# Performance work log

Measured on AMD Instinct MI355X. Metric: run time of the kernel, lower is better.

Reference implementation:

```python
import jax, jax.numpy as jnp
import numpy as np

B, T, D_HID, D_TRK, N_TRANS = 128, 40, 512, 256, 64


def setup_inputs() -> dict:
    key = jax.random.key(0)
    ks = jax.random.split(key, 8)
    d, t = D_HID, D_TRK
    s = 0.05
    return {
        "buffers": jax.random.normal(ks[0], (B, T, 2 * d), jnp.float32),
        "W_left": jax.random.normal(ks[1], (5 * d, d), jnp.float32) * s,
        "b_left": jnp.zeros((5 * d,), jnp.float32),
        "W_right": jax.random.normal(ks[2], (5 * d, d), jnp.float32) * s,
        "W_track": jax.random.normal(ks[3], (5 * d, t), jnp.float32) * s,
        "W_ih": jax.random.normal(ks[4], (4 * t, 3 * d), jnp.float32) * s,
        "W_hh": jax.random.normal(ks[5], (4 * t, t), jnp.float32) * s,
        "b_ih": jnp.zeros((4 * t,), jnp.float32),
        "b_hh": jnp.zeros((4 * t,), jnp.float32),
        "W_trans": jax.random.normal(ks[6], (4, t), jnp.float32) * s,
        "b_trans": jnp.zeros((4,), jnp.float32),
        "transitions": jax.random.randint(ks[7], (N_TRANS, B), 0, 4),
    }


def _spinn_forward(buffers, W_left, b_left, W_right, W_track,
                   W_ih, W_hh, b_ih, b_hh, W_trans, b_trans, n_steps):
    # Thin-stack style vectorized SPINN: fixed-capacity stack + pointers.
    Bb, Tt, two_d = buffers.shape
    d = two_d // 2
    t = W_hh.shape[1]
    cap = Tt + 2  # stack never exceeds 2 initial + (T-2) shifts
    dtype = buffers.dtype

    stack0 = jnp.zeros((Bb, cap, two_d), dtype)
    # stacks = [buf[0], buf[0]] in the torch code
    stack0 = stack0.at[:, 0].set(buffers[:, 0]).at[:, 1].set(buffers[:, 0])
    sptr0 = jnp.full((Bb,), 2, jnp.int32)   # stack length
    blen0 = jnp.full((Bb,), Tt, jnp.int32)  # buffer length (pops from the end)
    th0 = jnp.zeros((Bb, t), dtype)
    tc0 = jnp.zeros((Bb, t), dtype)
    bidx = jnp.arange(Bb)

    def step(carry, _):
        stack, sptr, blen, th, tc = carry
        buf_top = buffers[bidx, blen - 1]          # buf[-1], [B, 2d]
        s1 = stack[bidx, sptr - 1]                 # stack[-1]
        s2 = stack[bidx, sptr - 2]                 # stack[-2]
        # Tracker LSTMCell on cat(buf_h, stack1_h, stack2_h)
        x = jnp.concatenate([buf_top[:, :d], s1[:, :d], s2[:, :d]], axis=1)
        gates = x @ W_ih.T + b_ih + th @ W_hh.T + b_hh
        gi, gf, gg, go = jnp.split(gates, 4, axis=1)
        tc_new = jax.nn.sigmoid(gf) * tc + jax.nn.sigmoid(gi) * jnp.tanh(gg)
        th_new = jax.nn.sigmoid(go) * jnp.tanh(tc_new)
        logits = th_new @ W_trans.T + b_trans      # [B, 4]
        trans = jnp.argmax(logits, axis=1)
        do_shift = (trans == 3) & (blen > 2)
        do_red = (trans == 2) & (sptr > 3)
        # REDUCE (TreeLSTM) computed for all rows, masked in below.
        # left = stack[-2], right = stack[-1] (right popped first in torch).
        lstm_in = (s2[:, :d] @ W_left.T + b_left
                   + s1[:, :d] @ W_right.T
                   + th_new @ W_track.T)           # [B, 5d]
        a, i_, f1, f2, o_ = jnp.split(lstm_in, 5, axis=1)
        c = (jnp.tanh(a) * jax.nn.sigmoid(i_)
             + jax.nn.sigmoid(f1) * s2[:, d:]
             + jax.nn.sigmoid(f2) * s1[:, d:])
        h = jax.nn.sigmoid(o_) * jnp.tanh(c)
        node = jnp.concatenate([h, c], axis=1)
        # SHIFT: push buf_top; REDUCE: overwrite stack[-2] and shrink by 1.
        stack = stack.at[bidx, sptr].set(
            jnp.where(do_shift[:, None], buf_top, stack[bidx, sptr]))
        stack = stack.at[bidx, sptr - 2].set(
            jnp.where(do_red[:, None], node, stack[bidx, sptr - 2]))
        sptr = sptr + do_shift.astype(jnp.int32) - do_red.astype(jnp.int32)
        blen = blen - do_shift.astype(jnp.int32)
        return (stack, sptr, blen, th_new, tc_new), logits

    _, all_logits = jax.lax.scan(step, (stack0, sptr0, blen0, th0, tc0),
                                 None, length=n_steps)
    return all_logits  # [n_steps, B, 4] = stacked trans_preds_batch


def reference(buffers, W_left, b_left, W_right, W_track, W_ih, W_hh,
              b_ih, b_hh, W_trans, b_trans, transitions):
    n_steps = transitions.shape[0]  # torch only uses transitions.size(0)
    return _spinn_forward(buffers, W_left, b_left, W_right, W_track,
                          W_ih, W_hh, b_ih, b_hh, W_trans, b_trans, n_steps)
```

## Files before the change

### kernel.cpp

```cpp
#include <hip/hip_runtime.h>
#include <math.h>


#define B_ 128
#define CAP 40
#define XW 1536
#define GSPLIT 12
#define LSPLIT 8
#define NSTEP 64

__device__ __forceinline__ float sigm(float x) { return 1.f / (1.f + expf(-x)); }

__global__ void k_repack(const float* __restrict__ W_ih, const float* __restrict__ W_hh,
                         const float* __restrict__ W_left, const float* __restrict__ W_right,
                         const float* __restrict__ W_track, const float* __restrict__ b_ih,
                         const float* __restrict__ b_hh,
                         float* __restrict__ W1T, float* __restrict__ W2T,
                         float* __restrict__ W3T, float* __restrict__ WhhT,
                         float* __restrict__ b1) {
    size_t idx = (size_t)blockIdx.x * 256 + threadIdx.x;
    const size_t n1 = 1536ull * 1024ull;
    const size_t n2 = 1024ull * 2560ull;
    const size_t n3 = 256ull * 2560ull;
    const size_t n4 = 256ull * 1024ull;
    if (idx < n1) {
        int k = (int)(idx >> 10), n = (int)(idx & 1023);
        W1T[idx] = W_ih[(size_t)n * 1536 + k];
    } else if (idx < n1 + n2) {
        size_t r = idx - n1;
        int k = (int)(r / 2560), n = (int)(r % 2560);
        W2T[r] = (k < 512) ? W_right[(size_t)n * 512 + k] : W_left[(size_t)n * 512 + (k - 512)];
    } else if (idx < n1 + n2 + n3) {
        size_t r = idx - n1 - n2;
        int k = (int)(r / 2560), n = (int)(r % 2560);
        W3T[r] = W_track[(size_t)n * 256 + k];
    } else if (idx < n1 + n2 + n3 + n4) {
        size_t r = idx - n1 - n2 - n3;
        int k = (int)(r >> 10), n = (int)(r & 1023);
        WhhT[r] = W_hh[(size_t)n * 256 + k];
    } else if (idx < n1 + n2 + n3 + n4 + 1024) {
        int i = (int)(idx - n1 - n2 - n3 - n4);
        b1[i] = b_ih[i] + b_hh[i];
    }
}

__global__ void k_init(const float* __restrict__ buffers, float* __restrict__ stack,
                       float* __restrict__ X, float* __restrict__ tc,
                       float* __restrict__ hh,
                       int* __restrict__ sptr, int* __restrict__ blen) {
    int b = blockIdx.x, t = threadIdx.x;
    const float* b0 = buffers + (size_t)b * 40 * 1024;
    const float* btop = b0 + 39 * 1024;
    float* stk = stack + (size_t)b * CAP * 1024;
    for (int j = t; j < 1024; j += 256) { stk[j] = b0[j]; stk[1024 + j] = b0[j]; }
    float* Xb = X + (size_t)b * XW;
    for (int j = t; j < 512; j += 256) {
        Xb[j] = btop[j]; Xb[512 + j] = b0[j]; Xb[1024 + j] = b0[j];
    }
    tc[b * 256 + t] = 0.f;
    for (int j = t; j < 1024; j += 256) hh[(size_t)b * 1024 + j] = 0.f;
    if (t == 0) { sptr[b] = 2; blen[b] = 40; }
}

__global__ __launch_bounds__(256, 3) void k_gemm(const float* __restrict__ X,
                                                 const float* __restrict__ W1T,
                                                 const float* __restrict__ W2T,
                                                 float* __restrict__ gpart,
                                                 float* __restrict__ lpart) {
    __shared__ float As[32][132];
    __shared__ float Ws[32][68];
    const int bid = blockIdx.x;
    const float* WT; float* out; int N, n0, k0, aoff;
    if (bid < 192) {
        int ks = bid >> 4, nb = bid & 15;
        WT = W1T; out = gpart + (size_t)ks * 131072;
        N = 1024; n0 = nb * 64; k0 = ks * 128; aoff = 0;
    } else {
        int tI = bid - 192; int ks = tI / 40, nb = tI % 40;
        WT = W2T; out = lpart + (size_t)ks * 327680;
        N = 2560; n0 = nb * 64; k0 = ks * 128; aoff = 512;
    }
    const int tid = threadIdx.x;
    const int tm = tid >> 4;
    const int tn = tid & 15;

    float acc[8][4];
#pragma unroll
    for (int i = 0; i < 8; i++)
#pragma unroll
        for (int j = 0; j < 4; j++) acc[i][j] = 0.f;

    for (int ki = 0; ki < 128; ki += 32) {
        const int kb = k0 + ki;
        __syncthreads();
        {
            int m = tid >> 1;
            int c8 = (tid & 1) * 16;
            const float4* src = (const float4*)(X + (size_t)m * XW + aoff + kb + c8);
#pragma unroll
            for (int j = 0; j < 4; j++) {
                float4 v = src[j];
                int kk = c8 + j * 4;
                As[kk + 0][m] = v.x; As[kk + 1][m] = v.y; As[kk + 2][m] = v.z; As[kk + 3][m] = v.w;
            }
        }
        {
            int kk = tid >> 3;
            int c = (tid & 7) * 8;
            const float4* src = (const float4*)(WT + (size_t)(kb + kk) * N + n0 + c);
            float4* dst = (float4*)(&Ws[kk][c]);
            dst[0] = src[0]; dst[1] = src[1];
        }
        __syncthreads();
#pragma unroll 4
        for (int kk = 0; kk < 32; kk++) {
            float a[8], w[4];
            *(float4*)&a[0] = *(const float4*)&As[kk][tm * 4];
            *(float4*)&a[4] = *(const float4*)&As[kk][64 + tm * 4];
            *(float4*)&w[0] = *(const float4*)&Ws[kk][tn * 4];
#pragma unroll
            for (int i = 0; i < 8; i++)
#pragma unroll
                for (int j = 0; j < 4; j++) acc[i][j] += a[i] * w[j];
        }
    }
    float* base = out + n0 + tn * 4;
#pragma unroll
    for (int i = 0; i < 8; i++) {
        int m = (i < 4) ? (tm * 4 + i) : (64 + tm * 4 + (i - 4));
        *(float4*)(base + (size_t)m * N) = make_float4(acc[i][0], acc[i][1], acc[i][2], acc[i][3]);
    }
}

__global__ __launch_bounds__(256) void k_B(const float* __restrict__ gpart,
                                           const float* __restrict__ lpart,
                                           const float* __restrict__ hh_in,
                                           float* __restrict__ hh_out,
                                           const float* __restrict__ b1,
                                           const float* __restrict__ b_left,
                                           const float* __restrict__ W3T,
                                           const float* __restrict__ WhhT,
                                           const float* __restrict__ W_trans,
                                           const float* __restrict__ b_trans,
                                           const float* __restrict__ buffers,
                                           float* __restrict__ stack,
                                           float* __restrict__ X,
                                           const float* __restrict__ tc_in,
                                           float* __restrict__ tc_out,
                                           const int* __restrict__ sp_in,
                                           int* __restrict__ sp_out,
                                           const int* __restrict__ bl_in,
                                           int* __restrict__ bl_out,
                                           float* __restrict__ out_s) {
    const int bid = blockIdx.x;
    const int b = bid >> 2, q = bid & 3;
    const int t = threadIdx.x;
    const int sp = sp_in[b], bl = bl_in[b];
    __shared__ float sh_th[256];
    __shared__ float redw[4][4];
    __shared__ float shg[5][128];

    const float* gp = gpart + (size_t)b * 1024;
    const float* hp = hh_in + (size_t)b * 1024;
    float gi = b1[t] + hp[t],             gf = b1[256 + t] + hp[256 + t];
    float gg = b1[512 + t] + hp[512 + t], go = b1[768 + t] + hp[768 + t];
#pragma unroll 4
    for (int kc = 0; kc < GSPLIT; kc++) {
        const float* p = gp + (size_t)kc * 131072;
        gi += p[t]; gf += p[256 + t]; gg += p[512 + t]; go += p[768 + t];
    }
    float tcv = tc_in[b * 256 + t];
    float tcn = sigm(gf) * tcv + sigm(gi) * tanhf(gg);
    float thn = sigm(go) * tanhf(tcn);
    if ((t >> 6) == q) tc_out[b * 256 + t] = tcn;
    sh_th[t] = thn;

    float v0 = thn * W_trans[t],       v1 = thn * W_trans[256 + t];
    float v2 = thn * W_trans[512 + t], v3 = thn * W_trans[768 + t];
#pragma unroll
    for (int off = 32; off > 0; off >>= 1) {
        v0 += __shfl_down(v0, off); v1 += __shfl_down(v1, off);
        v2 += __shfl_down(v2, off); v3 += __shfl_down(v3, off);
    }
    if ((t & 63) == 0) {
        int w = t >> 6;
        redw[w][0] = v0; redw[w][1] = v1; redw[w][2] = v2; redw[w][3] = v3;
    }
    __syncthreads();
    float lg0 = redw[0][0] + redw[1][0] + redw[2][0] + redw[3][0] + b_trans[0];
    float lg1 = redw[0][1] + redw[1][1] + redw[2][1] + redw[3][1] + b_trans[1];
    float lg2 = redw[0][2] + redw[1][2] + redw[2][2] + redw[3][2] + b_trans[2];
    float lg3 = redw[0][3] + redw[1][3] + redw[2][3] + redw[3][3] + b_trans[3];
    int tr = 0; float best = lg0;
    if (lg1 > best) { best = lg1; tr = 1; }
    if (lg2 > best) { best = lg2; tr = 2; }
    if (lg3 > best) { best = lg3; tr = 3; }
    const bool do_shift = (tr == 3) && (bl > 2);
    const bool do_red   = (tr == 2) && (sp > 3);
    const int spn = sp + (do_shift ? 1 : 0) - (do_red ? 1 : 0);
    const int bln = bl - (do_shift ? 1 : 0);
    if (q == 0 && t == 0) {
        out_s[b * 4 + 0] = lg0; out_s[b * 4 + 1] = lg1;
        out_s[b * 4 + 2] = lg2; out_s[b * 4 + 3] = lg3;
        sp_out[b] = spn; bl_out[b] = bln;
    }
    float* stk = stack + (size_t)b * CAP * 1024;

    {
        const float* wh = WhhT + q * 256 + t;
        float h0 = 0, h1 = 0, h2 = 0, h3 = 0;
#pragma unroll 8
        for (int k = 0; k < 256; k += 4) {
            h0 += sh_th[k]     * wh[(size_t)k * 1024];
            h1 += sh_th[k + 1] * wh[(size_t)(k + 1) * 1024];
            h2 += sh_th[k + 2] * wh[(size_t)(k + 2) * 1024];
            h3 += sh_th[k + 3] * wh[(size_t)(k + 3) * 1024];
        }
        hh_out[(size_t)b * 1024 + q * 256 + t] = (h0 + h1) + (h2 + h3);
    }

    const int jj = t & 127, kh = t >> 7, j = q * 128 + jj;
    float node_h = 0.f;
    float a, ii, f1, f2, oo;
    if (do_red) {
        if (kh == 0) {
            a  = b_left[j];        ii = b_left[512 + j]; f1 = b_left[1024 + j];
            f2 = b_left[1536 + j]; oo = b_left[2048 + j];
        } else { a = ii = f1 = f2 = oo = 0.f; }
        const float* lp = lpart + (size_t)b * 2560;
        const int half = LSPLIT >> 1;
        for (int kc = kh * half; kc < kh * half + half; kc++) {
            const float* p = lp + (size_t)kc * 327680;
            a += p[j]; ii += p[512 + j]; f1 += p[1024 + j]; f2 += p[1536 + j]; oo += p[2048 + j];
        }
        const float* w = W3T + j;
#pragma unroll 4
        for (int k = kh * 128; k < kh * 128 + 128; k++) {
            float th = sh_th[k];
            const float* wk = w + (size_t)k * 2560;
            a += th * wk[0]; ii += th * wk[512]; f1 += th * wk[1024];
            f2 += th * wk[1536]; oo += th * wk[2048];
        }
        if (kh == 1) {
            shg[0][jj] = a; shg[1][jj] = ii; shg[2][jj] = f1; shg[3][jj] = f2; shg[4][jj] = oo;
        }
    }
    __syncthreads();
    if (do_red && kh == 0) {
        a += shg[0][jj]; ii += shg[1][jj]; f1 += shg[2][jj];
        f2 += shg[3][jj]; oo += shg[4][jj];
        float s1c = stk[(size_t)(sp - 1) * 1024 + 512 + j];
        float s2c = stk[(size_t)(sp - 2) * 1024 + 512 + j];
        float c = tanhf(a) * sigm(ii) + sigm(f1) * s2c + sigm(f2) * s1c;
        float h = sigm(oo) * tanhf(c);
        stk[(size_t)(sp - 2) * 1024 + j] = h;
        stk[(size_t)(sp - 2) * 1024 + 512 + j] = c;
        node_h = h;
    }
    if (do_shift) {
        const float* bt = buffers + ((size_t)b * 40 + (bl - 1)) * 1024;
        const int idx = q * 256 + t;
        stk[(size_t)sp * 1024 + idx] = bt[idx];
    }
    float* Xb = X + (size_t)b * XW;
    if (kh == 0) {
        const float* btn = buffers + ((size_t)b * 40 + (bln - 1)) * 1024;
        Xb[j] = btn[j];
        float s1h;
        if (do_red)        s1h = node_h;
        else if (do_shift) s1h = buffers[((size_t)b * 40 + (bl - 1)) * 1024 + j];
        else               s1h = stk[(size_t)(sp - 1) * 1024 + j];
        Xb[512 + j] = s1h;
        Xb[1024 + j] = stk[(size_t)(spn - 2) * 1024 + j];
    }
}

extern "C" void kernel_launch(void* const* d_in, const int* in_sizes, int n_in,
                              void* d_out, int out_size, void* d_ws, size_t ws_size,
                              hipStream_t stream) {
    const float* buffers = (const float*)d_in[0];
    const float* W_left  = (const float*)d_in[1];
    const float* b_left  = (const float*)d_in[2];
    const float* W_right = (const float*)d_in[3];
    const float* W_track = (const float*)d_in[4];
    const float* W_ih    = (const float*)d_in[5];
    const float* W_hh    = (const float*)d_in[6];
    const float* b_ih    = (const float*)d_in[7];
    const float* b_hh    = (const float*)d_in[8];
    const float* W_trans = (const float*)d_in[9];
    const float* b_trans = (const float*)d_in[10];
    float* out = (float*)d_out;

    float* ws = (float*)d_ws;
    size_t off = 0;
    float* W1T   = ws + off; off += 1536ull * 1024;
    float* W2T   = ws + off; off += 1024ull * 2560;
    float* W3T   = ws + off; off += 256ull * 2560;
    float* WhhT  = ws + off; off += 256ull * 1024;
    float* b1    = ws + off; off += 1024;
    float* X     = ws + off; off += (size_t)B_ * XW;
    float* tc_a  = ws + off; off += (size_t)B_ * 256;
    float* tc_b  = ws + off; off += (size_t)B_ * 256;
    float* hh_a  = ws + off; off += (size_t)B_ * 1024;
    float* hh_b  = ws + off; off += (size_t)B_ * 1024;
    float* gpart = ws + off; off += (size_t)GSPLIT * 131072;
    float* lpart = ws + off; off += (size_t)LSPLIT * 327680;
    float* stack = ws + off; off += (size_t)B_ * CAP * 1024;
    int* sp_a = (int*)(ws + off); off += 128;
    int* sp_b = (int*)(ws + off); off += 128;
    int* bl_a = (int*)(ws + off); off += 128;
    int* bl_b = (int*)(ws + off); off += 128;

    {
        size_t total = 1536ull * 1024 + 1024ull * 2560 + 256ull * 2560 + 256ull * 1024 + 1024;
        int blocks = (int)((total + 255) / 256);
        k_repack<<<blocks, 256, 0, stream>>>(W_ih, W_hh, W_left, W_right, W_track, b_ih, b_hh,
                                             W1T, W2T, W3T, WhhT, b1);
        k_init<<<B_, 256, 0, stream>>>(buffers, stack, X, tc_a, hh_a, sp_a, bl_a);
    }

    for (int s = 0; s < NSTEP; s++) {
        k_gemm<<<512, 256, 0, stream>>>(X, W1T, W2T, gpart, lpart);
        const float* tci = (s & 1) ? tc_b : tc_a;  float* tco = (s & 1) ? tc_a : tc_b;
        const float* hhi = (s & 1) ? hh_b : hh_a;  float* hho = (s & 1) ? hh_a : hh_b;
        const int*   spi = (s & 1) ? sp_b : sp_a;  int*   spo = (s & 1) ? sp_a : sp_b;
        const int*   bli = (s & 1) ? bl_b : bl_a;  int*   blo = (s & 1) ? bl_a : bl_b;
        k_B<<<512, 256, 0, stream>>>(gpart, lpart, hhi, hho, b1, b_left, W3T, WhhT,
                                     W_trans, b_trans, buffers, stack, X, tci, tco,
                                     spi, spo, bli, blo, out + (size_t)s * B_ * 4);
    }
    (void)in_sizes; (void)n_in; (void)out_size; (void)ws_size;
}
```

Baseline: 2.472 ms.

## Use untransposed W_track/W_hh in step kernel and enlarge GEMM per-thread tile

The W_track and W_hh transposes are dropped from the repack kernel. The step kernel now reads the original row-major weights with per-thread float4 loads along k instead of strided column reads. This removes repack work and workspace, but each thread now walks its own row, so neighbouring lanes touch addresses 1KB apart and coalescing is lost. Separately, the GEMM kernel drops to 128 threads, each computing an 8x8 tile instead of 8x4, which raises register reuse but halves the threads per block.

```diff
diff --git a/kernel.cpp b/kernel.cpp
--- a/kernel.cpp
+++ b/kernel.cpp
@@ -11,18 +11,14 @@
 
 __device__ __forceinline__ float sigm(float x) { return 1.f / (1.f + expf(-x)); }
 
-__global__ void k_repack(const float* __restrict__ W_ih, const float* __restrict__ W_hh,
+__global__ void k_repack(const float* __restrict__ W_ih,
                          const float* __restrict__ W_left, const float* __restrict__ W_right,
-                         const float* __restrict__ W_track, const float* __restrict__ b_ih,
-                         const float* __restrict__ b_hh,
+                         const float* __restrict__ b_ih, const float* __restrict__ b_hh,
                          float* __restrict__ W1T, float* __restrict__ W2T,
-                         float* __restrict__ W3T, float* __restrict__ WhhT,
                          float* __restrict__ b1) {
     size_t idx = (size_t)blockIdx.x * 256 + threadIdx.x;
     const size_t n1 = 1536ull * 1024ull;
     const size_t n2 = 1024ull * 2560ull;
-    const size_t n3 = 256ull * 2560ull;
-    const size_t n4 = 256ull * 1024ull;
     if (idx < n1) {
         int k = (int)(idx >> 10), n = (int)(idx & 1023);
         W1T[idx] = W_ih[(size_t)n * 1536 + k];
@@ -30,16 +26,8 @@
         size_t r = idx - n1;
         int k = (int)(r / 2560), n = (int)(r % 2560);
         W2T[r] = (k < 512) ? W_right[(size_t)n * 512 + k] : W_left[(size_t)n * 512 + (k - 512)];
-    } else if (idx < n1 + n2 + n3) {
-        size_t r = idx - n1 - n2;
-        int k = (int)(r / 2560), n = (int)(r % 2560);
-        W3T[r] = W_track[(size_t)n * 256 + k];
-    } else if (idx < n1 + n2 + n3 + n4) {
-        size_t r = idx - n1 - n2 - n3;
-        int k = (int)(r >> 10), n = (int)(r & 1023);
-        WhhT[r] = W_hh[(size_t)n * 256 + k];
-    } else if (idx < n1 + n2 + n3 + n4 + 1024) {
-        int i = (int)(idx - n1 - n2 - n3 - n4);
+    } else if (idx < n1 + n2 + 1024) {
+        int i = (int)(idx - n1 - n2);
         b1[i] = b_ih[i] + b_hh[i];
     }
 }
@@ -62,7 +50,7 @@
     if (t == 0) { sptr[b] = 2; blen[b] = 40; }
 }
 
-__global__ __launch_bounds__(256, 3) void k_gemm(const float* __restrict__ X,
+__global__ __launch_bounds__(128, 1) void k_gemm(const float* __restrict__ X,
                                                  const float* __restrict__ W1T,
                                                  const float* __restrict__ W2T,
                                                  float* __restrict__ gpart,
@@ -81,14 +69,14 @@
         N = 2560; n0 = nb * 64; k0 = ks * 128; aoff = 512;
     }
     const int tid = threadIdx.x;
-    const int tm = tid >> 4;
-    const int tn = tid & 15;
-
-    float acc[8][4];
+    const int tm = tid >> 3;
+    const int tn = tid & 7;
+
+    float acc[8][8];
 #pragma unroll
     for (int i = 0; i < 8; i++)
 #pragma unroll
-        for (int j = 0; j < 4; j++) acc[i][j] = 0.f;
+        for (int j = 0; j < 8; j++) acc[i][j] = 0.f;
 
     for (int ki = 0; ki < 128; ki += 32) {
         const int kb = k0 + ki;
@@ -96,39 +84,50 @@
         {
             int m = tid >> 1;
             int c8 = (tid & 1) * 16;
-            const float4* src = (const float4*)(X + (size_t)m * XW + aoff + kb + c8);
+            const float4* s0 = (const float4*)(X + (size_t)m * XW + aoff + kb + c8);
+            const float4* s1 = (const float4*)(X + (size_t)(m + 64) * XW + aoff + kb + c8);
 #pragma unroll
             for (int j = 0; j < 4; j++) {
-                float4 v = src[j];
+                float4 v = s0[j];
                 int kk = c8 + j * 4;
                 As[kk + 0][m] = v.x; As[kk + 1][m] = v.y; As[kk + 2][m] = v.z; As[kk + 3][m] = v.w;
             }
+#pragma unroll
+            for (int j = 0; j < 4; j++) {
+                float4 v = s1[j];
+                int kk = c8 + j * 4;
+                As[kk + 0][m + 64] = v.x; As[kk + 1][m + 64] = v.y;
+                As[kk + 2][m + 64] = v.z; As[kk + 3][m + 64] = v.w;
+            }
         }
         {
-            int kk = tid >> 3;
-            int c = (tid & 7) * 8;
+            int kk = tid >> 2;
+            int c = (tid & 3) * 16;
             const float4* src = (const float4*)(WT + (size_t)(kb + kk) * N + n0 + c);
             float4* dst = (float4*)(&Ws[kk][c]);
-            dst[0] = src[0]; dst[1] = src[1];
+            dst[0] = src[0]; dst[1] = src[1]; dst[2] = src[2]; dst[3] = src[3];
         }
         __syncthreads();
 #pragma unroll 4
         for (int kk = 0; kk < 32; kk++) {
-            float a[8], w[4];
+            float a[8], w[8];
             *(float4*)&a[0] = *(const float4*)&As[kk][tm * 4];
             *(float4*)&a[4] = *(const float4*)&As[kk][64 + tm * 4];
             *(float4*)&w[0] = *(const float4*)&Ws[kk][tn * 4];
+            *(float4*)&w[4] = *(const float4*)&Ws[kk][32 + tn * 4];
 #pragma unroll
             for (int i = 0; i < 8; i++)
 #pragma unroll
-                for (int j = 0; j < 4; j++) acc[i][j] += a[i] * w[j];
-        }
-    }
-    float* base = out + n0 + tn * 4;
+                for (int j = 0; j < 8; j++) acc[i][j] += a[i] * w[j];
+        }
+    }
+    float* base = out + n0;
 #pragma unroll
     for (int i = 0; i < 8; i++) {
         int m = (i < 4) ? (tm * 4 + i) : (64 + tm * 4 + (i - 4));
-        *(float4*)(base + (size_t)m * N) = make_float4(acc[i][0], acc[i][1], acc[i][2], acc[i][3]);
+        float* p = base + (size_t)m * N;
+        *(float4*)(p + tn * 4)      = make_float4(acc[i][0], acc[i][1], acc[i][2], acc[i][3]);
+        *(float4*)(p + 32 + tn * 4) = make_float4(acc[i][4], acc[i][5], acc[i][6], acc[i][7]);
     }
 }
 
@@ -138,8 +137,8 @@
                                            float* __restrict__ hh_out,
                                            const float* __restrict__ b1,
                                            const float* __restrict__ b_left,
-                                           const float* __restrict__ W3T,
-                                           const float* __restrict__ WhhT,
+                                           const float* __restrict__ W_track,
+                                           const float* __restrict__ W_hh,
                                            const float* __restrict__ W_trans,
                                            const float* __restrict__ b_trans,
                                            const float* __restrict__ buffers,
@@ -207,14 +206,15 @@
     float* stk = stack + (size_t)b * CAP * 1024;
 
     {
-        const float* wh = WhhT + q * 256 + t;
+        const float* wh = W_hh + (size_t)(q * 256 + t) * 256;
         float h0 = 0, h1 = 0, h2 = 0, h3 = 0;
 #pragma unroll 8
         for (int k = 0; k < 256; k += 4) {
-            h0 += sh_th[k]     * wh[(size_t)k * 1024];
-            h1 += sh_th[k + 1] * wh[(size_t)(k + 1) * 1024];
-            h2 += sh_th[k + 2] * wh[(size_t)(k + 2) * 1024];
-            h3 += sh_th[k + 3] * wh[(size_t)(k + 3) * 1024];
+            float4 w = *(const float4*)(wh + k);
+            h0 += sh_th[k]     * w.x;
+            h1 += sh_th[k + 1] * w.y;
+            h2 += sh_th[k + 2] * w.z;
+            h3 += sh_th[k + 3] * w.w;
         }
         hh_out[(size_t)b * 1024 + q * 256 + t] = (h0 + h1) + (h2 + h3);
     }
@@ -233,13 +233,22 @@
             const float* p = lp + (size_t)kc * 327680;
             a += p[j]; ii += p[512 + j]; f1 += p[1024 + j]; f2 += p[1536 + j]; oo += p[2048 + j];
         }
-        const float* w = W3T + j;
+        const int kb = kh * 128;
+        const float* wa = W_track + (size_t)j * 256 + kb;
+        const float* wi = W_track + (size_t)(512 + j) * 256 + kb;
+        const float* w1 = W_track + (size_t)(1024 + j) * 256 + kb;
+        const float* w2 = W_track + (size_t)(1536 + j) * 256 + kb;
+        const float* wo = W_track + (size_t)(2048 + j) * 256 + kb;
+        const float* ths = &sh_th[kb];
 #pragma unroll 4
-        for (int k = kh * 128; k < kh * 128 + 128; k++) {
-            float th = sh_th[k];
-            const float* wk = w + (size_t)k * 2560;
-            a += th * wk[0]; ii += th * wk[512]; f1 += th * wk[1024];
-            f2 += th * wk[1536]; oo += th * wk[2048];
+        for (int k = 0; k < 128; k += 4) {
+            float t0 = ths[k], t1 = ths[k + 1], t2 = ths[k + 2], t3 = ths[k + 3];
+            float4 w;
+            w = *(const float4*)(wa + k); a  += t0 * w.x; a  += t1 * w.y; a  += t2 * w.z; a  += t3 * w.w;
+            w = *(const float4*)(wi + k); ii += t0 * w.x; ii += t1 * w.y; ii += t2 * w.z; ii += t3 * w.w;
+            w = *(const float4*)(w1 + k); f1 += t0 * w.x; f1 += t1 * w.y; f1 += t2 * w.z; f1 += t3 * w.w;
+            w = *(const float4*)(w2 + k); f2 += t0 * w.x; f2 += t1 * w.y; f2 += t2 * w.z; f2 += t3 * w.w;
+            w = *(const float4*)(wo + k); oo += t0 * w.x; oo += t1 * w.y; oo += t2 * w.z; oo += t3 * w.w;
         }
         if (kh == 1) {
             shg[0][jj] = a; shg[1][jj] = ii; shg[2][jj] = f1; shg[3][jj] = f2; shg[4][jj] = oo;
@@ -295,8 +304,6 @@
     size_t off = 0;
     float* W1T   = ws + off; off += 1536ull * 1024;
     float* W2T   = ws + off; off += 1024ull * 2560;
-    float* W3T   = ws + off; off += 256ull * 2560;
-    float* WhhT  = ws + off; off += 256ull * 1024;
     float* b1    = ws + off; off += 1024;
     float* X     = ws + off; off += (size_t)B_ * XW;
     float* tc_a  = ws + off; off += (size_t)B_ * 256;
@@ -312,20 +319,20 @@
     int* bl_b = (int*)(ws + off); off += 128;
 
     {
-        size_t total = 1536ull * 1024 + 1024ull * 2560 + 256ull * 2560 + 256ull * 1024 + 1024;
+        size_t total = 1536ull * 1024 + 1024ull * 2560 + 1024;
         int blocks = (int)((total + 255) / 256);
-        k_repack<<<blocks, 256, 0, stream>>>(W_ih, W_hh, W_left, W_right, W_track, b_ih, b_hh,
-                                             W1T, W2T, W3T, WhhT, b1);
+        k_repack<<<blocks, 256, 0, stream>>>(W_ih, W_left, W_right, b_ih, b_hh,
+                                             W1T, W2T, b1);
         k_init<<<B_, 256, 0, stream>>>(buffers, stack, X, tc_a, hh_a, sp_a, bl_a);
     }
 
     for (int s = 0; s < NSTEP; s++) {
-        k_gemm<<<512, 256, 0, stream>>>(X, W1T, W2T, gpart, lpart);
+        k_gemm<<<512, 128, 0, stream>>>(X, W1T, W2T, gpart, lpart);
         const float* tci = (s & 1) ? tc_b : tc_a;  float* tco = (s & 1) ? tc_a : tc_b;
         const float* hhi = (s & 1) ? hh_b : hh_a;  float* hho = (s & 1) ? hh_a : hh_b;
         const int*   spi = (s & 1) ? sp_b : sp_a;  int*   spo = (s & 1) ? sp_a : sp_b;
         const int*   bli = (s & 1) ? bl_b : bl_a;  int*   blo = (s & 1) ? bl_a : bl_b;
-        k_B<<<512, 256, 0, stream>>>(gpart, lpart, hhi, hho, b1, b_left, W3T, WhhT,
+        k_B<<<512, 256, 0, stream>>>(gpart, lpart, hhi, hho, b1, b_left, W_track, W_hh,
                                      W_trans, b_trans, buffers, stack, X, tci, tco,
                                      spi, spo, bli, blo, out + (size_t)s * B_ * 4);
     }
```

New measurement: 3.694 ms. +49.4%, slower.

## Interleave small weight matrices by k-quads and stream GEMM weights from global

Applied to the files above, without the earlier changes.

The tracker and hidden-to-hidden weights are repacked so that four consecutive k values per column sit together, letting k_B fetch them with float4 loads instead of scalar strided loads. In k_gemm the shared-memory staging tile for weights is removed: each thread reads its float4 of weights straight from global memory, while the activation tile grows to 64 k-rows per sync to halve barrier count. Launch bounds drop from 3 to 2 blocks per CU to make room for the larger LDS tile. The risk is that direct global weight reads lose the reuse and coalescing that LDS provided, and lower occupancy may hide latency less well.

```diff
diff --git a/kernel.cpp b/kernel.cpp
--- a/kernel.cpp
+++ b/kernel.cpp
@@ -16,13 +16,13 @@
                          const float* __restrict__ W_track, const float* __restrict__ b_ih,
                          const float* __restrict__ b_hh,
                          float* __restrict__ W1T, float* __restrict__ W2T,
-                         float* __restrict__ W3T, float* __restrict__ WhhT,
+                         float* __restrict__ W3T4, float* __restrict__ WhhT4,
                          float* __restrict__ b1) {
     size_t idx = (size_t)blockIdx.x * 256 + threadIdx.x;
     const size_t n1 = 1536ull * 1024ull;
     const size_t n2 = 1024ull * 2560ull;
-    const size_t n3 = 256ull * 2560ull;
-    const size_t n4 = 256ull * 1024ull;
+    const size_t n3 = 64ull * 2560ull * 4ull;
+    const size_t n4 = 64ull * 1024ull * 4ull;
     if (idx < n1) {
         int k = (int)(idx >> 10), n = (int)(idx & 1023);
         W1T[idx] = W_ih[(size_t)n * 1536 + k];
@@ -32,12 +32,16 @@
         W2T[r] = (k < 512) ? W_right[(size_t)n * 512 + k] : W_left[(size_t)n * 512 + (k - 512)];
     } else if (idx < n1 + n2 + n3) {
         size_t r = idx - n1 - n2;
-        int k = (int)(r / 2560), n = (int)(r % 2560);
-        W3T[r] = W_track[(size_t)n * 256 + k];
+        int k4 = (int)(r / 10240);
+        int rem = (int)(r % 10240);
+        int col = rem >> 2, i = rem & 3;
+        W3T4[r] = W_track[(size_t)col * 256 + k4 * 4 + i];
     } else if (idx < n1 + n2 + n3 + n4) {
         size_t r = idx - n1 - n2 - n3;
-        int k = (int)(r >> 10), n = (int)(r & 1023);
-        WhhT[r] = W_hh[(size_t)n * 256 + k];
+        int k4 = (int)(r >> 12);
+        int rem = (int)(r & 4095);
+        int n = rem >> 2, i = rem & 3;
+        WhhT4[r] = W_hh[(size_t)n * 256 + k4 * 4 + i];
     } else if (idx < n1 + n2 + n3 + n4 + 1024) {
         int i = (int)(idx - n1 - n2 - n3 - n4);
         b1[i] = b_ih[i] + b_hh[i];
@@ -62,13 +66,12 @@
     if (t == 0) { sptr[b] = 2; blen[b] = 40; }
 }
 
-__global__ __launch_bounds__(256, 3) void k_gemm(const float* __restrict__ X,
+__global__ __launch_bounds__(256, 2) void k_gemm(const float* __restrict__ X,
                                                  const float* __restrict__ W1T,
                                                  const float* __restrict__ W2T,
                                                  float* __restrict__ gpart,
                                                  float* __restrict__ lpart) {
-    __shared__ float As[32][132];
-    __shared__ float Ws[32][68];
+    __shared__ float As[64][132];
     const int bid = blockIdx.x;
     const float* WT; float* out; int N, n0, k0, aoff;
     if (bid < 192) {
@@ -90,34 +93,28 @@
 #pragma unroll
         for (int j = 0; j < 4; j++) acc[i][j] = 0.f;
 
-    for (int ki = 0; ki < 128; ki += 32) {
+    for (int ki = 0; ki < 128; ki += 64) {
         const int kb = k0 + ki;
         __syncthreads();
         {
             int m = tid >> 1;
-            int c8 = (tid & 1) * 16;
-            const float4* src = (const float4*)(X + (size_t)m * XW + aoff + kb + c8);
-#pragma unroll
-            for (int j = 0; j < 4; j++) {
+            int c0 = (tid & 1) * 32;
+            const float4* src = (const float4*)(X + (size_t)m * XW + aoff + kb + c0);
+#pragma unroll
+            for (int j = 0; j < 8; j++) {
                 float4 v = src[j];
-                int kk = c8 + j * 4;
+                int kk = c0 + j * 4;
                 As[kk + 0][m] = v.x; As[kk + 1][m] = v.y; As[kk + 2][m] = v.z; As[kk + 3][m] = v.w;
             }
         }
-        {
-            int kk = tid >> 3;
-            int c = (tid & 7) * 8;
-            const float4* src = (const float4*)(WT + (size_t)(kb + kk) * N + n0 + c);
-            float4* dst = (float4*)(&Ws[kk][c]);
-            dst[0] = src[0]; dst[1] = src[1];
-        }
         __syncthreads();
-#pragma unroll 4
-        for (int kk = 0; kk < 32; kk++) {
+        const float* wp = WT + (size_t)kb * N + n0 + tn * 4;
+#pragma unroll 8
+        for (int kk = 0; kk < 64; kk++) {
             float a[8], w[4];
             *(float4*)&a[0] = *(const float4*)&As[kk][tm * 4];
             *(float4*)&a[4] = *(const float4*)&As[kk][64 + tm * 4];
-            *(float4*)&w[0] = *(const float4*)&Ws[kk][tn * 4];
+            *(float4*)&w[0] = *(const float4*)(wp + (size_t)kk * N);
 #pragma unroll
             for (int i = 0; i < 8; i++)
 #pragma unroll
@@ -138,8 +135,8 @@
                                            float* __restrict__ hh_out,
                                            const float* __restrict__ b1,
                                            const float* __restrict__ b_left,
-                                           const float* __restrict__ W3T,
-                                           const float* __restrict__ WhhT,
+                                           const float* __restrict__ W3T4,
+                                           const float* __restrict__ WhhT4,
                                            const float* __restrict__ W_trans,
                                            const float* __restrict__ b_trans,
                                            const float* __restrict__ buffers,
@@ -207,14 +204,15 @@
     float* stk = stack + (size_t)b * CAP * 1024;
 
     {
-        const float* wh = WhhT + q * 256 + t;
+        const float* wh = WhhT4 + (size_t)(q * 256 + t) * 4;
         float h0 = 0, h1 = 0, h2 = 0, h3 = 0;
 #pragma unroll 8
-        for (int k = 0; k < 256; k += 4) {
-            h0 += sh_th[k]     * wh[(size_t)k * 1024];
-            h1 += sh_th[k + 1] * wh[(size_t)(k + 1) * 1024];
-            h2 += sh_th[k + 2] * wh[(size_t)(k + 2) * 1024];
-            h3 += sh_th[k + 3] * wh[(size_t)(k + 3) * 1024];
+        for (int k4 = 0; k4 < 64; k4++) {
+            float4 w = *(const float4*)(wh + (size_t)k4 * 4096);
+            h0 += sh_th[4 * k4]     * w.x;
+            h1 += sh_th[4 * k4 + 1] * w.y;
+            h2 += sh_th[4 * k4 + 2] * w.z;
+            h3 += sh_th[4 * k4 + 3] * w.w;
         }
         hh_out[(size_t)b * 1024 + q * 256 + t] = (h0 + h1) + (h2 + h3);
     }
@@ -233,13 +231,18 @@
             const float* p = lp + (size_t)kc * 327680;
             a += p[j]; ii += p[512 + j]; f1 += p[1024 + j]; f2 += p[1536 + j]; oo += p[2048 + j];
         }
-        const float* w = W3T + j;
+        const float* w = W3T4 + (size_t)j * 4;
 #pragma unroll 4
-        for (int k = kh * 128; k < kh * 128 + 128; k++) {
-            float th = sh_th[k];
-            const float* wk = w + (size_t)k * 2560;
-            a += th * wk[0]; ii += th * wk[512]; f1 += th * wk[1024];
-            f2 += th * wk[1536]; oo += th * wk[2048];
+        for (int k4 = kh * 32; k4 < kh * 32 + 32; k4++) {
+            float t0 = sh_th[4 * k4],     t1 = sh_th[4 * k4 + 1];
+            float t2 = sh_th[4 * k4 + 2], t3 = sh_th[4 * k4 + 3];
+            const float* wk = w + (size_t)k4 * 10240;
+            float4 wv;
+            wv = *(const float4*)(wk);        a  += t0 * wv.x; a  += t1 * wv.y; a  += t2 * wv.z; a  += t3 * wv.w;
+            wv = *(const float4*)(wk + 2048); ii += t0 * wv.x; ii += t1 * wv.y; ii += t2 * wv.z; ii += t3 * wv.w;
+            wv = *(const float4*)(wk + 4096); f1 += t0 * wv.x; f1 += t1 * wv.y; f1 += t2 * wv.z; f1 += t3 * wv.w;
+            wv = *(const float4*)(wk + 6144); f2 += t0 * wv.x; f2 += t1 * wv.y; f2 += t2 * wv.z; f2 += t3 * wv.w;
+            wv = *(const float4*)(wk + 8192); oo += t0 * wv.x; oo += t1 * wv.y; oo += t2 * wv.z; oo += t3 * wv.w;
         }
         if (kh == 1) {
             shg[0][jj] = a; shg[1][jj] = ii; shg[2][jj] = f1; shg[3][jj] = f2; shg[4][jj] = oo;
@@ -295,8 +298,8 @@
     size_t off = 0;
     float* W1T   = ws + off; off += 1536ull * 1024;
     float* W2T   = ws + off; off += 1024ull * 2560;
-    float* W3T   = ws + off; off += 256ull * 2560;
-    float* WhhT  = ws + off; off += 256ull * 1024;
+    float* W3T4  = ws + off; off += 64ull * 2560 * 4;
+    float* WhhT4 = ws + off; off += 64ull * 1024 * 4;
     float* b1    = ws + off; off += 1024;
     float* X     = ws + off; off += (size_t)B_ * XW;
     float* tc_a  = ws + off; off += (size_t)B_ * 256;
@@ -312,10 +315,11 @@
     int* bl_b = (int*)(ws + off); off += 128;
 
     {
-        size_t total = 1536ull * 1024 + 1024ull * 2560 + 256ull * 2560 + 256ull * 1024 + 1024;
+        size_t total = 1536ull * 1024 + 1024ull * 2560 + 64ull * 2560 * 4
+                     + 64ull * 1024 * 4 + 1024;
         int blocks = (int)((total + 255) / 256);
         k_repack<<<blocks, 256, 0, stream>>>(W_ih, W_hh, W_left, W_right, W_track, b_ih, b_hh,
-                                             W1T, W2T, W3T, WhhT, b1);
+                                             W1T, W2T, W3T4, WhhT4, b1);
         k_init<<<B_, 256, 0, stream>>>(buffers, stack, X, tc_a, hh_a, sp_a, bl_a);
     }
 
@@ -325,7 +329,7 @@
         const float* hhi = (s & 1) ? hh_b : hh_a;  float* hho = (s & 1) ? hh_a : hh_b;
         const int*   spi = (s & 1) ? sp_b : sp_a;  int*   spo = (s & 1) ? sp_a : sp_b;
         const int*   bli = (s & 1) ? bl_b : bl_a;  int*   blo = (s & 1) ? bl_a : bl_b;
-        k_B<<<512, 256, 0, stream>>>(gpart, lpart, hhi, hho, b1, b_left, W3T, WhhT,
+        k_B<<<512, 256, 0, stream>>>(gpart, lpart, hhi, hho, b1, b_left, W3T4, WhhT4,
                                      W_trans, b_trans, buffers, stack, X, tci, tco,
                                      spi, spo, bli, blo, out + (size_t)s * B_ * 4);
     }
```

After: 4.029 ms. 63.0% more time.
